# Kernel optimization log

Measured on AMD Instinct MI355X. Metric: run time of the kernel, lower is better.

## Reference

```python
import jax, jax.numpy as jnp
import numpy as np

N_NODES = 50000
N_EDGES = 800000
IN_F = 128
HEADS = 4
OUT_F = 16  # per-head channels; concat output = HEADS*OUT_F = 64
NEG_SLOPE = 0.2


def setup_inputs() -> dict:
    key = jax.random.key(0)
    ks = jax.random.split(key, 9)
    x = jax.random.normal(ks[0], (N_NODES, IN_F), dtype=jnp.float32)
    edge_index = jax.random.randint(ks[1], (2, N_EDGES), 0, N_NODES, dtype=jnp.int64)
    edge_attr = jax.random.normal(ks[2], (N_EDGES, 1), dtype=jnp.float32)
    s = 1.0 / np.sqrt(IN_F)
    W = jax.random.normal(ks[3], (IN_F, HEADS * OUT_F), dtype=jnp.float32) * s
    W_edge = jax.random.normal(ks[4], (1, HEADS * OUT_F), dtype=jnp.float32)
    att_src = jax.random.normal(ks[5], (HEADS, OUT_F), dtype=jnp.float32) * s
    att_dst = jax.random.normal(ks[6], (HEADS, OUT_F), dtype=jnp.float32) * s
    att_edge = jax.random.normal(ks[7], (HEADS, OUT_F), dtype=jnp.float32) * s
    bias = jax.random.normal(ks[8], (HEADS * OUT_F,), dtype=jnp.float32) * 0.01
    return {"x": x, "edge_index": edge_index, "edge_attr": edge_attr,
            "W": W, "W_edge": W_edge, "att_src": att_src,
            "att_dst": att_dst, "att_edge": att_edge, "bias": bias}


def reference(x, edge_index, edge_attr, W, W_edge, att_src, att_dst, att_edge, bias):
    N = x.shape[0]
    H, C = att_src.shape
    src, dst = edge_index[0], edge_index[1]

    # add_self_loops with fill_value='mean': per-dst mean of incoming edge_attr
    deg = jax.ops.segment_sum(jnp.ones_like(edge_attr[:, 0]), dst, num_segments=N)
    ea_mean = jax.ops.segment_sum(edge_attr, dst, num_segments=N) / jnp.maximum(deg, 1.0)[:, None]
    loop = jnp.arange(N, dtype=src.dtype)
    src_f = jnp.concatenate([src, loop])   # [E+N]
    dst_f = jnp.concatenate([dst, loop])
    ea = jnp.concatenate([edge_attr, ea_mean], axis=0)  # [E+N, 1]

    # node transform + per-node attention logits
    xw = (x @ W).reshape(N, H, C)                 # [N,H,C]
    a_src = jnp.einsum('nhc,hc->nh', xw, att_src)  # [N,H]
    a_dst = jnp.einsum('nhc,hc->nh', xw, att_dst)

    # edge feature transform + edge logits
    ew = (ea @ W_edge).reshape(-1, H, C)           # [E+N,H,C]
    a_edge = jnp.einsum('ehc,hc->eh', ew, att_edge)

    # gather, LeakyReLU, segment softmax over incoming edges per dst node
    alpha = jax.nn.leaky_relu(a_src[src_f] + a_dst[dst_f] + a_edge, NEG_SLOPE)  # [E+N,H]
    amax = jax.ops.segment_max(alpha, dst_f, num_segments=N)                    # [N,H]
    ex = jnp.exp(alpha - amax[dst_f])
    denom = jax.ops.segment_sum(ex, dst_f, num_segments=N)
    att = ex / denom[dst_f]                                                     # [E+N,H]

    # weighted scatter-aggregate of source messages
    msg = xw[src_f] * att[:, :, None]                       # [E+N,H,C]
    out = jax.ops.segment_sum(msg, dst_f, num_segments=N)    # [N,H,C]
    out = out.reshape(N, H * C) + bias

    # batchnorm=Identity, dropout in eval mode; activation=relu
    return jax.nn.relu(out)
```

## Files before the change

kernel.cpp:

```cpp
#include <hip/hip_runtime.h>
#include <hip/hip_fp16.h>
#include <math.h>

#define NN 50000
#define NE 800000
#define INF_ 128
#define HEADS 4
#define OUTF 16
#define HC 64
#define NEG_SLOPE 0.2f
#define NBKT 196
#define CAP 5120
#define CHA 4096
#define NBA ((NE + CHA - 1) / CHA)
#define WPB 4
#define XPAD 136

typedef _Float16 half8 __attribute__((ext_vector_type(8)));
typedef float f32x4 __attribute__((ext_vector_type(4)));

__device__ __forceinline__ unsigned short h2u(float f) {
    __half h = __float2half(f);
    return *(unsigned short*)&h;
}
__device__ __forceinline__ float u2f(unsigned short u) {
    __half h = *(__half*)&u;
    return __half2float(h);
}
__device__ __forceinline__ float lrelu(float v) {
    return v > 0.f ? v : NEG_SLOPE * v;
}

__global__ __launch_bounds__(256) void k_xw(
    const float* __restrict__ x, const float* __restrict__ W,
    const float* __restrict__ att_src, const float* __restrict__ att_dst,
    unsigned short* __restrict__ xw16, unsigned short* __restrict__ a_src16,
    float* __restrict__ a_dst) {
    __shared__ _Float16 sxh[64][XPAD];
    __shared__ _Float16 sWT[64][XPAD];
    int t = threadIdx.x;
    int n0 = blockIdx.x * 64;
    for (int i = t; i < 64 * 32; i += 256) {
        int r = i >> 5, c4 = (i & 31) * 4;
        int n = n0 + r;
        float4 v = (n < NN) ? *(const float4*)&x[(size_t)n * INF_ + c4]
                            : make_float4(0.f, 0.f, 0.f, 0.f);
        sxh[r][c4 + 0] = (_Float16)v.x;
        sxh[r][c4 + 1] = (_Float16)v.y;
        sxh[r][c4 + 2] = (_Float16)v.z;
        sxh[r][c4 + 3] = (_Float16)v.w;
    }
    for (int i = t; i < INF_ * HC; i += 256) {
        int k = i >> 6, c = i & 63;
        sWT[c][k] = (_Float16)W[i];
    }
    __syncthreads();
    int w = t >> 6, l = t & 63;
    int lr = l & 15, kg = l >> 4;
    f32x4 acc0 = {0.f,0.f,0.f,0.f}, acc1 = acc0, acc2 = acc0, acc3 = acc0;
#pragma unroll
    for (int kk = 0; kk < 4; ++kk) {
        half8 a = *(half8*)&sxh[w * 16 + lr][kk * 32 + kg * 8];
        half8 b0 = *(half8*)&sWT[0 * 16 + lr][kk * 32 + kg * 8];
        half8 b1 = *(half8*)&sWT[1 * 16 + lr][kk * 32 + kg * 8];
        half8 b2 = *(half8*)&sWT[2 * 16 + lr][kk * 32 + kg * 8];
        half8 b3 = *(half8*)&sWT[3 * 16 + lr][kk * 32 + kg * 8];
        acc0 = __builtin_amdgcn_mfma_f32_16x16x32_f16(a, b0, acc0, 0, 0, 0);
        acc1 = __builtin_amdgcn_mfma_f32_16x16x32_f16(a, b1, acc1, 0, 0, 0);
        acc2 = __builtin_amdgcn_mfma_f32_16x16x32_f16(a, b2, acc2, 0, 0, 0);
        acc3 = __builtin_amdgcn_mfma_f32_16x16x32_f16(a, b3, acc3, 0, 0, 0);
    }
    float attS[4], attD[4];
#pragma unroll
    for (int ct = 0; ct < 4; ++ct) {
        attS[ct] = att_src[ct * 16 + lr];
        attD[ct] = att_dst[ct * 16 + lr];
    }
    int rbase = n0 + w * 16 + kg * 4;
    f32x4 accs[4] = {acc0, acc1, acc2, acc3};
#pragma unroll
    for (int ct = 0; ct < 4; ++ct) {
#pragma unroll
        for (int j = 0; j < 4; ++j) {
            float c = accs[ct][j];
            int node = rbase + j;
            if (node < NN)
                xw16[(size_t)node * HC + ct * 16 + lr] = h2u(c);
            float vs = c * attS[ct];
            float vd = c * attD[ct];
#pragma unroll
            for (int m = 1; m < 16; m <<= 1) {
                vs += __shfl_xor(vs, m);
                vd += __shfl_xor(vd, m);
            }
            if (lr == 0 && node < NN) {
                a_src16[node * HEADS + ct] = h2u(vs);
                a_dst[node * HEADS + ct] = vd;
            }
        }
    }
}

__global__ __launch_bounds__(256) void k_binA(const int* __restrict__ ei,
                                              const float* __restrict__ ea,
                                              int* __restrict__ ccur,
                                              uint2* __restrict__ ebuf) {
    __shared__ int lh[NBKT], lcur[NBKT];
    int t = threadIdx.x;
    int e0 = blockIdx.x * CHA;
    int ecnt = NE - e0; if (ecnt > CHA) ecnt = CHA;
    for (int i = t; i < NBKT; i += 256) lh[i] = 0;
    __syncthreads();
    if (ecnt == CHA) {
        int dl[16];
#pragma unroll
        for (int j = 0; j < 16; ++j) {
            dl[j] = ei[NE + e0 + t + j * 256];
            atomicAdd(&lh[dl[j] >> 8], 1);
        }
        __syncthreads();
        for (int i = t; i < NBKT; i += 256)
            lcur[i] = lh[i] ? (i * CAP + atomicAdd(&ccur[i], lh[i])) : 0;
        __syncthreads();
#pragma unroll
        for (int j = 0; j < 16; ++j) {
            int e = e0 + t + j * 256;
            int dst = dl[j];
            int b = dst >> 8;
            int p = atomicAdd(&lcur[b], 1);
            if (p < (b + 1) * CAP) {
                uint2 pk;
                pk.x = (unsigned)ei[e] | ((unsigned)(dst & 255) << 16);
                pk.y = __float_as_uint(ea[e]);
                ebuf[p] = pk;
            }
        }
    } else {
        for (int i = t; i < ecnt; i += 256)
            atomicAdd(&lh[ei[NE + e0 + i] >> 8], 1);
        __syncthreads();
        for (int i = t; i < NBKT; i += 256)
            lcur[i] = lh[i] ? (i * CAP + atomicAdd(&ccur[i], lh[i])) : 0;
        __syncthreads();
        for (int i = t; i < ecnt; i += 256) {
            int e = e0 + i;
            int dst = ei[NE + e];
            int b = dst >> 8;
            int p = atomicAdd(&lcur[b], 1);
            if (p < (b + 1) * CAP) {
                uint2 pk;
                pk.x = (unsigned)ei[e] | ((unsigned)(dst & 255) << 16);
                pk.y = __float_as_uint(ea[e]);
                ebuf[p] = pk;
            }
        }
    }
}

__global__ __launch_bounds__(256) void k_binB(const int* __restrict__ ccur,
                                              const uint2* __restrict__ ebuf,
                                              unsigned* __restrict__ esort,
                                              int* __restrict__ deg,
                                              int* __restrict__ offs,
                                              float* __restrict__ easum) {
    __shared__ int lh[256], lcur[256], sd[256];
    __shared__ float lsum[256];
    int t = threadIdx.x;
    int b = blockIdx.x;
    int base = b * CAP;
    int cnt = ccur[b]; if (cnt > CAP) cnt = CAP;
    lh[t] = 0;
    lsum[t] = 0.f;
    __syncthreads();
    for (int i = t; i < cnt; i += 256)
        atomicAdd(&lh[(ebuf[base + i].x >> 16) & 255], 1);
    __syncthreads();
    int v = lh[t];
    sd[t] = v; __syncthreads();
    for (int o = 1; o < 256; o <<= 1) {
        int a = (t >= o) ? sd[t - o] : 0;
        __syncthreads();
        sd[t] += a;
        __syncthreads();
    }
    int ex = sd[t] - v;
    lcur[t] = ex;
    __syncthreads();
    for (int i = t; i < cnt; i += 256) {
        uint2 pk = ebuf[base + i];
        int d = (pk.x >> 16) & 255;
        int p = atomicAdd(&lcur[d], 1);
        atomicAdd(&lsum[d], __uint_as_float(pk.y));
        esort[base + p] = (pk.x & 0xFFFFu) |
                          ((unsigned)h2u(__uint_as_float(pk.y)) << 16);
    }
    __syncthreads();
    int n = (b << 8) + t;
    if (n < NN) { deg[n] = v; offs[n] = base + ex; easum[n] = lsum[t]; }
}

__global__ __launch_bounds__(256) void k_gather(
    const unsigned* __restrict__ esort, const int* __restrict__ offs,
    const int* __restrict__ deg, const float* __restrict__ easum,
    const unsigned short* __restrict__ a_src16, const float* __restrict__ a_dst,
    const unsigned short* __restrict__ xw16,
    const float* __restrict__ W_edge, const float* __restrict__ att_edge,
    const float* __restrict__ bias, float* __restrict__ out) {
    __shared__ __align__(16) float sce[4];
    __shared__ __align__(16) float ldsP[WPB][16][4];
    __shared__ int ldsS[WPB][16];
    int t = threadIdx.x;
    if (t < 4) {
        float s_ = 0.f;
        for (int k = 0; k < OUTF; ++k)
            s_ = fmaf(W_edge[t * OUTF + k], att_edge[t * OUTF + k], s_);
        sce[t] = s_;
    }
    __syncthreads();
    int lane = t & 63;
    int wslot = t >> 6;
    int n = (blockIdx.x << 2) + wslot;
    int e16 = lane & 15;
    int h = lane >> 4;

    float ceh = sce[h];
    float adh = a_dst[n * HEADS + h];
    int start = offs[n];
    int cnt = deg[n];

    float s = 0.f, acc = 0.f;

    int nch = (cnt + 15) >> 4;
    for (int ch = 0; ch < nch; ++ch) {
        int base = start + (ch << 4);
        int cc = cnt - (ch << 4); if (cc > 16) cc = 16;
        bool valid = e16 < cc;
        unsigned se = esort[base + e16];
        int srci = (int)(se & 0xFFFFu);
        float eav = u2f((unsigned short)(se >> 16));
        float asv = u2f(a_src16[srci * HEADS + h]);
        float p = 0.f;
        if (valid) p = __expf(lrelu(asv + adh + eav * ceh));
        ldsP[wslot][e16][h] = p;
        if (h == 0) ldsS[wslot][e16] = srci;
        asm volatile("s_waitcnt lgkmcnt(0)" ::: "memory");
        __builtin_amdgcn_sched_barrier(0);
#pragma unroll 4
        for (int i = 0; i < cc; ++i) {
            float pv = ldsP[wslot][i][h];
            int si = ldsS[wslot][i];
            float xv = u2f(xw16[(size_t)si * HC + lane]);
            s += pv;
            acc = fmaf(pv, xv, acc);
        }
        asm volatile("s_waitcnt lgkmcnt(0)" ::: "memory");
        __builtin_amdgcn_sched_barrier(0);
    }
    float asn = u2f(a_src16[n * HEADS + h]);
    float eavm = easum[n] / fmaxf((float)cnt, 1.f);
    float p = __expf(lrelu(asn + adh + eavm * ceh));
    float xself = u2f(xw16[(size_t)n * HC + lane]);
    s += p;
    acc = fmaf(p, xself, acc);
    out[(size_t)n * HC + lane] = fmaxf(acc / s + bias[lane], 0.f);
}

extern "C" void kernel_launch(void* const* d_in, const int* in_sizes, int n_in,
                              void* d_out, int out_size, void* d_ws, size_t ws_size,
                              hipStream_t stream) {
    const float* x        = (const float*)d_in[0];
    const int*   ei       = (const int*)d_in[1];
    const float* ea       = (const float*)d_in[2];
    const float* W        = (const float*)d_in[3];
    const float* W_edge   = (const float*)d_in[4];
    const float* att_src  = (const float*)d_in[5];
    const float* att_dst  = (const float*)d_in[6];
    const float* att_edge = (const float*)d_in[7];
    const float* bias     = (const float*)d_in[8];
    float* out = (float*)d_out;

    float* ws = (float*)d_ws;
    unsigned short* xw16    = (unsigned short*)ws;
    uint2* ebuf   = (uint2*)(ws + (size_t)32 * NN);
    unsigned* esort = (unsigned*)(ebuf + (size_t)NBKT * CAP + 64);
    unsigned short* a_src16 = (unsigned short*)(esort + (size_t)NBKT * CAP + 64);
    float* a_dst  = (float*)(a_src16 + (size_t)HEADS * NN);
    int*   deg    = (int*)(a_dst + (size_t)HEADS * NN);
    int*   offs   = deg + NN;
    float* easum  = (float*)(offs + NN);
    int*   ccur   = (int*)(easum + NN);

    hipMemsetAsync(ccur, 0, NBKT * sizeof(int), stream);
    k_binA<<<NBA, 256, 0, stream>>>(ei, ea, ccur, ebuf);
    k_binB<<<NBKT, 256, 0, stream>>>(ccur, ebuf, esort, deg, offs, easum);
    k_xw<<<(NN + 63) / 64, 256, 0, stream>>>(x, W, att_src, att_dst, xw16, a_src16, a_dst);
    k_gather<<<NN / 4, 256, 0, stream>>>(
        esort, offs, deg, easum, a_src16, a_dst, xw16, W_edge, att_edge, bias, out);
}
```

Baseline: 165.7 us.

## Merge binning and node transform into one launch; process two edges per wave in gather

The edge-binning kernel and the node transform kernel are combined into a single launch, with block ranges deciding which job each block does. The two are independent, so they can now run concurrently and one launch overhead goes away. In the gather, each half-wave handles a different edge and every lane loads two packed fp16 features at once, with the halves combined by a cross-lane shuffle at the end. This halves the serial per-edge loop iterations and widens the loads, at the cost of higher LDS usage in the fused kernel and an extra reduction step.

```diff
diff --git a/kernel.cpp b/kernel.cpp
--- a/kernel.cpp
+++ b/kernel.cpp
@@ -13,6 +13,7 @@
 #define CAP 5120
 #define CHA 4096
 #define NBA ((NE + CHA - 1) / CHA)
+#define NXW ((NN + 63) / 64)
 #define WPB 4
 #define XPAD 136
 
@@ -31,15 +32,69 @@
     return v > 0.f ? v : NEG_SLOPE * v;
 }
 
-__global__ __launch_bounds__(256) void k_xw(
+__global__ __launch_bounds__(256) void k_binA_xw(
+    const int* __restrict__ ei, const float* __restrict__ ea,
+    int* __restrict__ ccur, uint2* __restrict__ ebuf,
     const float* __restrict__ x, const float* __restrict__ W,
     const float* __restrict__ att_src, const float* __restrict__ att_dst,
     unsigned short* __restrict__ xw16, unsigned short* __restrict__ a_src16,
     float* __restrict__ a_dst) {
+    __shared__ int lh[NBKT], lcur[NBKT];
     __shared__ _Float16 sxh[64][XPAD];
     __shared__ _Float16 sWT[64][XPAD];
     int t = threadIdx.x;
-    int n0 = blockIdx.x * 64;
+    if (blockIdx.x < NBA) {
+        int e0 = blockIdx.x * CHA;
+        int ecnt = NE - e0; if (ecnt > CHA) ecnt = CHA;
+        for (int i = t; i < NBKT; i += 256) lh[i] = 0;
+        __syncthreads();
+        if (ecnt == CHA) {
+            int dl[16];
+#pragma unroll
+            for (int j = 0; j < 16; ++j) {
+                dl[j] = ei[NE + e0 + t + j * 256];
+                atomicAdd(&lh[dl[j] >> 8], 1);
+            }
+            __syncthreads();
+            for (int i = t; i < NBKT; i += 256)
+                lcur[i] = lh[i] ? (i * CAP + atomicAdd(&ccur[i], lh[i])) : 0;
+            __syncthreads();
+#pragma unroll
+            for (int j = 0; j < 16; ++j) {
+                int e = e0 + t + j * 256;
+                int dst = dl[j];
+                int b = dst >> 8;
+                int p = atomicAdd(&lcur[b], 1);
+                if (p < (b + 1) * CAP) {
+                    uint2 pk;
+                    pk.x = (unsigned)ei[e] | ((unsigned)(dst & 255) << 16);
+                    pk.y = __float_as_uint(ea[e]);
+                    ebuf[p] = pk;
+                }
+            }
+        } else {
+            for (int i = t; i < ecnt; i += 256)
+                atomicAdd(&lh[ei[NE + e0 + i] >> 8], 1);
+            __syncthreads();
+            for (int i = t; i < NBKT; i += 256)
+                lcur[i] = lh[i] ? (i * CAP + atomicAdd(&ccur[i], lh[i])) : 0;
+            __syncthreads();
+            for (int i = t; i < ecnt; i += 256) {
+                int e = e0 + i;
+                int dst = ei[NE + e];
+                int b = dst >> 8;
+                int p = atomicAdd(&lcur[b], 1);
+                if (p < (b + 1) * CAP) {
+                    uint2 pk;
+                    pk.x = (unsigned)ei[e] | ((unsigned)(dst & 255) << 16);
+                    pk.y = __float_as_uint(ea[e]);
+                    ebuf[p] = pk;
+                }
+            }
+        }
+        return;
+    }
+    int n0 = (blockIdx.x - NBA) * 64;
     for (int i = t; i < 64 * 32; i += 256) {
         int r = i >> 5, c4 = (i & 31) * 4;
         int n = n0 + r;
@@ -96,62 +151,6 @@
             if (lr == 0 && node < NN) {
                 a_src16[node * HEADS + ct] = h2u(vs);
                 a_dst[node * HEADS + ct] = vd;
-            }
-        }
-    }
-}
-
-__global__ __launch_bounds__(256) void k_binA(const int* __restrict__ ei,
-                                              const float* __restrict__ ea,
-                                              int* __restrict__ ccur,
-                                              uint2* __restrict__ ebuf) {
-    __shared__ int lh[NBKT], lcur[NBKT];
-    int t = threadIdx.x;
-    int e0 = blockIdx.x * CHA;
-    int ecnt = NE - e0; if (ecnt > CHA) ecnt = CHA;
-    for (int i = t; i < NBKT; i += 256) lh[i] = 0;
-    __syncthreads();
-    if (ecnt == CHA) {
-        int dl[16];
-#pragma unroll
-        for (int j = 0; j < 16; ++j) {
-            dl[j] = ei[NE + e0 + t + j * 256];
-            atomicAdd(&lh[dl[j] >> 8], 1);
-        }
-        __syncthreads();
-        for (int i = t; i < NBKT; i += 256)
-            lcur[i] = lh[i] ? (i * CAP + atomicAdd(&ccur[i], lh[i])) : 0;
-        __syncthreads();
-#pragma unroll
-        for (int j = 0; j < 16; ++j) {
-            int e = e0 + t + j * 256;
-            int dst = dl[j];
-            int b = dst >> 8;
-            int p = atomicAdd(&lcur[b], 1);
-            if (p < (b + 1) * CAP) {
-                uint2 pk;
-                pk.x = (unsigned)ei[e] | ((unsigned)(dst & 255) << 16);
-                pk.y = __float_as_uint(ea[e]);
-                ebuf[p] = pk;
-            }
-        }
-    } else {
-        for (int i = t; i < ecnt; i += 256)
-            atomicAdd(&lh[ei[NE + e0 + i] >> 8], 1);
-        __syncthreads();
-        for (int i = t; i < NBKT; i += 256)
-            lcur[i] = lh[i] ? (i * CAP + atomicAdd(&ccur[i], lh[i])) : 0;
-        __syncthreads();
-        for (int i = t; i < ecnt; i += 256) {
-            int e = e0 + i;
-            int dst = ei[NE + e];
-            int b = dst >> 8;
-            int p = atomicAdd(&lcur[b], 1);
-            if (p < (b + 1) * CAP) {
-                uint2 pk;
-                pk.x = (unsigned)ei[e] | ((unsigned)(dst & 255) << 16);
-                pk.y = __float_as_uint(ea[e]);
-                ebuf[p] = pk;
             }
         }
     }
@@ -220,15 +219,16 @@
     int lane = t & 63;
     int wslot = t >> 6;
     int n = (blockIdx.x << 2) + wslot;
-    int e16 = lane & 15;
-    int h = lane >> 4;
+    int e16 = lane & 15, h = lane >> 4;
+    int l32 = lane & 31, g = lane >> 5;
+    int c2 = l32 * 2, h2 = l32 >> 3;
 
     float ceh = sce[h];
     float adh = a_dst[n * HEADS + h];
     int start = offs[n];
     int cnt = deg[n];
 
-    float s = 0.f, acc = 0.f;
+    float s = 0.f, a0 = 0.f, a1 = 0.f;
 
     int nch = (cnt + 15) >> 4;
     for (int ch = 0; ch < nch; ++ch) {
@@ -246,23 +246,37 @@
         asm volatile("s_waitcnt lgkmcnt(0)" ::: "memory");
         __builtin_amdgcn_sched_barrier(0);
 #pragma unroll 4
-        for (int i = 0; i < cc; ++i) {
-            float pv = ldsP[wslot][i][h];
-            int si = ldsS[wslot][i];
-            float xv = u2f(xw16[(size_t)si * HC + lane]);
-            s += pv;
-            acc = fmaf(pv, xv, acc);
+        for (int i = 0; i < cc; i += 2) {
+            int ii = i + g;
+            if (ii < cc) {
+                float pv = ldsP[wslot][ii][h2];
+                int si = ldsS[wslot][ii];
+                unsigned xv = *(const unsigned*)&xw16[(size_t)si * HC + c2];
+                s += pv;
+                a0 = fmaf(pv, u2f((unsigned short)(xv & 0xFFFFu)), a0);
+                a1 = fmaf(pv, u2f((unsigned short)(xv >> 16)), a1);
+            }
         }
         asm volatile("s_waitcnt lgkmcnt(0)" ::: "memory");
         __builtin_amdgcn_sched_barrier(0);
     }
-    float asn = u2f(a_src16[n * HEADS + h]);
+    s  += __shfl_xor(s, 32);
+    a0 += __shfl_xor(a0, 32);
+    a1 += __shfl_xor(a1, 32);
+    float adB = a_dst[n * HEADS + h2];
+    float asnB = u2f(a_src16[n * HEADS + h2]);
     float eavm = easum[n] / fmaxf((float)cnt, 1.f);
-    float p = __expf(lrelu(asn + adh + eavm * ceh));
-    float xself = u2f(xw16[(size_t)n * HC + lane]);
-    s += p;
-    acc = fmaf(p, xself, acc);
-    out[(size_t)n * HC + lane] = fmaxf(acc / s + bias[lane], 0.f);
+    float pp = __expf(lrelu(asnB + adB + eavm * sce[h2]));
+    unsigned xs = *(const unsigned*)&xw16[(size_t)n * HC + c2];
+    s += pp;
+    a0 = fmaf(pp, u2f((unsigned short)(xs & 0xFFFFu)), a0);
+    a1 = fmaf(pp, u2f((unsigned short)(xs >> 16)), a1);
+    if (g == 0) {
+        float2 o;
+        o.x = fmaxf(a0 / s + bias[c2], 0.f);
+        o.y = fmaxf(a1 / s + bias[c2 + 1], 0.f);
+        *(float2*)&out[(size_t)n * HC + c2] = o;
+    }
 }
 
 extern "C" void kernel_launch(void* const* d_in, const int* in_sizes, int n_in,
@@ -291,9 +305,10 @@
     int*   ccur   = (int*)(easum + NN);
 
     hipMemsetAsync(ccur, 0, NBKT * sizeof(int), stream);
-    k_binA<<<NBA, 256, 0, stream>>>(ei, ea, ccur, ebuf);
+    k_binA_xw<<<NBA + NXW, 256, 0, stream>>>(ei, ea, ccur, ebuf,
+                                             x, W, att_src, att_dst,
+                                             xw16, a_src16, a_dst);
     k_binB<<<NBKT, 256, 0, stream>>>(ccur, ebuf, esort, deg, offs, easum);
-    k_xw<<<(NN + 63) / 64, 256, 0, stream>>>(x, W, att_src, att_dst, xw16, a_src16, a_dst);
     k_gather<<<NN / 4, 256, 0, stream>>>(
         esort, offs, deg, easum, a_src16, a_dst, xw16, W_edge, att_edge, bias, out);
 }
```

Result: faster. 162.3 us (-2.1%).
